# Performance work log

Hardware: AMD Instinct MI355X
Metric: run time of the kernel (lower is better)

Reference implementation:

```python
import jax, jax.numpy as jnp
import numpy as np

N = 100000  # nodes
E = 1600000  # edges


def _gcn_norm(edge_index, num_nodes):
    # PyG GCNConv default: add self-loops, symmetric normalization.
    src, dst = edge_index[0], edge_index[1]
    loop = jnp.arange(num_nodes, dtype=src.dtype)
    src = jnp.concatenate([src, loop])
    dst = jnp.concatenate([dst, loop])
    deg = jax.ops.segment_sum(jnp.ones_like(dst, dtype=jnp.float32), dst,
                              num_segments=num_nodes)
    dinv = jnp.where(deg > 0, jax.lax.rsqrt(deg), 0.0)
    norm = dinv[src] * dinv[dst]  # [E + N]
    return src, dst, norm


def _gcn_layer(x, W, b, src, dst, norm, num_nodes):
    h = x @ W                                # [N, out]
    msg = h[src] * norm[:, None]             # gather + scale, [E+N, out]
    agg = jax.ops.segment_sum(msg, dst, num_segments=num_nodes)
    return agg + b


def setup_inputs() -> dict:
    key = jax.random.key(0)
    ks = jax.random.split(key, 8)
    d_in, d_h, d_out = 128, 128, 64
    x = jax.random.normal(ks[0], (N, d_in), dtype=jnp.float32)
    edge_index = jax.random.randint(ks[1], (2, E), 0, N, dtype=jnp.int64)
    def glorot(k, fan_in, fan_out):
        s = jnp.sqrt(6.0 / (fan_in + fan_out)).astype(jnp.float32)
        return jax.random.uniform(k, (fan_in, fan_out), jnp.float32, -s, s)
    return {
        "x": x,
        "edge_index": edge_index,
        "W1": glorot(ks[2], d_in, d_h), "b1": jnp.zeros((d_h,), jnp.float32),
        "W2": glorot(ks[3], d_h, d_h), "b2": jnp.zeros((d_h,), jnp.float32),
        "W3": glorot(ks[4], d_h, d_out), "b3": jnp.zeros((d_out,), jnp.float32),
    }


def reference(x, edge_index, W1, b1, W2, b2, W3, b3):
    src, dst, norm = _gcn_norm(edge_index, N)
    h = jax.nn.relu(_gcn_layer(x, W1, b1, src, dst, norm, N))
    h = jax.nn.relu(_gcn_layer(h, W2, b2, src, dst, norm, N))
    h = jax.nn.relu(_gcn_layer(h, W3, b3, src, dst, norm, N))
    return h
```

## Files before the change

### kernel.cpp

```cpp
#include <hip/hip_runtime.h>
#include <hip/hip_bf16.h>
#include <hip/hip_fp16.h>


constexpr int N_NODES = 100000;
constexpr int E_EDGES = 1600000;
constexpr int SCAN_B = (N_NODES + 1023) / 1024;

typedef short short8 __attribute__((ext_vector_type(8)));
typedef float f32x4 __attribute__((ext_vector_type(4)));

__global__ __launch_bounds__(256) void rank_kernel(
    const int* __restrict__ dst, int* __restrict__ cnt,
    int* __restrict__ eRank) {
  int e = blockIdx.x * 256 + threadIdx.x;
  if (e < E_EDGES) eRank[e] = atomicAdd(&cnt[dst[e]], 1);
}

__global__ __launch_bounds__(256) void scan_part_kernel(
    const int* __restrict__ cnt, int* __restrict__ bsum) {
  __shared__ int red[256];
  const int t = threadIdx.x;
  int base = blockIdx.x * 1024 + t * 4;
  int4 v = make_int4(0, 0, 0, 0);
  if (base < N_NODES) v = *(const int4*)(cnt + base);
  red[t] = v.x + v.y + v.z + v.w;
  __syncthreads();
  for (int off = 128; off > 0; off >>= 1) {
    if (t < off) red[t] += red[t + off];
    __syncthreads();
  }
  if (t == 0) bsum[blockIdx.x] = red[0];
}

__global__ __launch_bounds__(128) void scan_tops_kernel(
    const int* __restrict__ bsum, int* __restrict__ boff,
    int* __restrict__ rowptr) {
  __shared__ int part[128];
  const int t = threadIdx.x;
  int v = (t < SCAN_B) ? bsum[t] : 0;
  part[t] = v;
  __syncthreads();
  for (int off = 1; off < 128; off <<= 1) {
    int add = (t >= off) ? part[t - off] : 0;
    __syncthreads();
    part[t] += add;
    __syncthreads();
  }
  if (t < SCAN_B) boff[t] = part[t] - v;
  if (t == 127) rowptr[N_NODES] = part[127];
}

__global__ __launch_bounds__(256) void scan_write_kernel(
    const int* __restrict__ cnt, const int* __restrict__ boff,
    int* __restrict__ rowptr, float* __restrict__ dinv) {
  __shared__ int part[256];
  const int t = threadIdx.x;
  int base = blockIdx.x * 1024 + t * 4;
  int4 v = make_int4(0, 0, 0, 0);
  if (base < N_NODES) v = *(const int4*)(cnt + base);
  int s = v.x + v.y + v.z + v.w;
  part[t] = s;
  __syncthreads();
  for (int off = 1; off < 256; off <<= 1) {
    int add = (t >= off) ? part[t - off] : 0;
    __syncthreads();
    part[t] += add;
    __syncthreads();
  }
  if (base < N_NODES) {
    int run = boff[blockIdx.x] + part[t] - s;
    int4 o;
    o.x = run;
    o.y = run + v.x;
    o.z = run + v.x + v.y;
    o.w = run + v.x + v.y + v.z;
    *(int4*)(rowptr + base) = o;
    float4 dv;
    dv.x = rsqrtf((float)v.x + 1.0f);
    dv.y = rsqrtf((float)v.y + 1.0f);
    dv.z = rsqrtf((float)v.z + 1.0f);
    dv.w = rsqrtf((float)v.w + 1.0f);
    *(float4*)(dinv + base) = dv;
  }
}

__global__ __launch_bounds__(256) void place_kernel(
    const int* __restrict__ src, const int* __restrict__ dst,
    const int* __restrict__ eRank, const int* __restrict__ rowptr,
    const float* __restrict__ dinv, int2* __restrict__ eSW) {
  int e = blockIdx.x * 256 + threadIdx.x;
  if (e < E_EDGES) {
    int d = dst[e];
    int s = src[e];
    int pos = rowptr[d] + eRank[e];
    eSW[pos] = make_int2(s, __float_as_int(dinv[s] * dinv[d]));
  }
}

__device__ inline ushort bf_round(float x) {
  uint u = __float_as_uint(x);
  return (ushort)((u + 0x7FFFu + ((u >> 16) & 1u)) >> 16);
}
__device__ inline ushort bf_split(float x, float* rem) {
  ushort h = bf_round(x);
  *rem = x - __uint_as_float((uint)h << 16);
  return h;
}

__device__ inline void packw_body(int id, int OC, const float* __restrict__ W,
                                  ushort* __restrict__ hi,
                                  ushort* __restrict__ lo) {
  if (id >= OC * 16) return;
  int col = id & 15;
  int g = (id >> 4) & 3;
  int ks = (id >> 6) & 3;
  int nt = id >> 8;
  int k0 = ks * 32 + g * 8;
  int n = nt * 16 + col;
  ushort h8[8], l8[8];
#pragma unroll
  for (int j = 0; j < 8; ++j) {
    float rem;
    h8[j] = bf_split(W[(size_t)(k0 + j) * OC + n], &rem);
    l8[j] = bf_round(rem);
  }
  size_t base = (size_t)id * 8;
#pragma unroll
  for (int j = 0; j < 8; ++j) {
    hi[base + j] = h8[j];
    lo[base + j] = l8[j];
  }
}

__global__ __launch_bounds__(256) void packw_all_kernel(
    const float* __restrict__ W1, ushort* __restrict__ h1,
    ushort* __restrict__ l1, const float* __restrict__ W2,
    ushort* __restrict__ h2, ushort* __restrict__ l2,
    const float* __restrict__ W3, ushort* __restrict__ h3,
    ushort* __restrict__ l3) {
  int b = blockIdx.x;
  if (b < 8) packw_body(b * 256 + threadIdx.x, 128, W1, h1, l1);
  else if (b < 16) packw_body((b - 8) * 256 + threadIdx.x, 128, W2, h2, l2);
  else packw_body((b - 16) * 256 + threadIdx.x, 64, W3, h3, l3);
}

template <int OC, bool HALF_IN>
__global__ __launch_bounds__(256) void gemm_kernel(
    const void* __restrict__ Xv, const ushort* __restrict__ Whi,
    const ushort* __restrict__ Wlo, __half* __restrict__ H) {
  constexpr int NT = OC / 16;
  __shared__ ushort sWhi[OC * 128];
  __shared__ ushort sWlo[OC * 128];
  const int t = threadIdx.x;
  {
    const uint4* gh = (const uint4*)Whi;
    const uint4* gl = (const uint4*)Wlo;
    uint4* sh = (uint4*)sWhi;
    uint4* sl = (uint4*)sWlo;
    for (int i = t; i < OC * 128 / 8; i += 256) {
      sh[i] = gh[i];
      sl[i] = gl[i];
    }
  }
  const int wid = t >> 6;
  const int lane = t & 63;
  const int bid = blockIdx.x;
  const int row = bid * 64 + wid * 16 + (lane & 15);
  const bool ok = row < N_NODES;
  const int g = lane >> 4;

  short8 ahi[4], alo[4];
#pragma unroll
  for (int ks = 0; ks < 4; ++ks) {
    float f[8];
    if (ok) {
      if constexpr (HALF_IN) {
        const __half* xr = (const __half*)Xv + (size_t)row * 128;
        uint4 u = *(const uint4*)(xr + ks * 32 + g * 8);
        float2 t0 = __half22float2(*(__half2*)&u.x);
        float2 t1 = __half22float2(*(__half2*)&u.y);
        float2 t2 = __half22float2(*(__half2*)&u.z);
        float2 t3 = __half22float2(*(__half2*)&u.w);
        f[0] = t0.x; f[1] = t0.y; f[2] = t1.x; f[3] = t1.y;
        f[4] = t2.x; f[5] = t2.y; f[6] = t3.x; f[7] = t3.y;
      } else {
        const float* xr = (const float*)Xv + (size_t)row * 128;
        float4 f0 = *(const float4*)(xr + ks * 32 + g * 8);
        float4 f1 = *(const float4*)(xr + ks * 32 + g * 8 + 4);
        f[0] = f0.x; f[1] = f0.y; f[2] = f0.z; f[3] = f0.w;
        f[4] = f1.x; f[5] = f1.y; f[6] = f1.z; f[7] = f1.w;
      }
    } else {
#pragma unroll
      for (int j = 0; j < 8; ++j) f[j] = 0.f;
    }
    union { short8 v; ushort u[8]; } h, l;
#pragma unroll
    for (int j = 0; j < 8; ++j) {
      float rem;
      h.u[j] = bf_split(f[j], &rem);
      l.u[j] = bf_round(rem);
    }
    ahi[ks] = h.v;
    alo[ks] = l.v;
  }
  __syncthreads();

#pragma unroll
  for (int nt = 0; nt < NT; ++nt) {
    f32x4 acc = {0.f, 0.f, 0.f, 0.f};
#pragma unroll
    for (int ks = 0; ks < 4; ++ks) {
      int off = (((nt * 4 + ks) * 4 + g) * 16 + (lane & 15)) * 8;
      short8 bhi = *(const short8*)&sWhi[off];
      short8 blo = *(const short8*)&sWlo[off];
      acc = __builtin_amdgcn_mfma_f32_16x16x32_bf16(alo[ks], bhi, acc, 0, 0, 0);
      acc = __builtin_amdgcn_mfma_f32_16x16x32_bf16(ahi[ks], blo, acc, 0, 0, 0);
      acc = __builtin_amdgcn_mfma_f32_16x16x32_bf16(ahi[ks], bhi, acc, 0, 0, 0);
    }
#pragma unroll
    for (int r = 0; r < 4; ++r) {
      int rr = bid * 64 + wid * 16 + g * 4 + r;
      if (rr < N_NODES)
        H[(size_t)rr * OC + nt * 16 + (lane & 15)] = __float2half(acc[r]);
    }
  }
}

template <int OC, bool HALF_OUT>
__global__ __launch_bounds__(256) void agg_kernel(
    const __half* __restrict__ H, const int* __restrict__ rowptr,
    const int2* __restrict__ eSW, const float* __restrict__ dinv,
    const float* __restrict__ bias, void* __restrict__ out) {
  const int wave = threadIdx.x >> 6;
  const int lane = threadIdx.x & 63;
  const int n = blockIdx.x * 4 + wave;
  if (n >= N_NODES) return;
  const float dn = dinv[n];
  const float selfw = dn * dn;
  const int beg = rowptr[n], end = rowptr[n + 1];
  const int jal = min(beg + (beg & 1), end);
  const int jend = jal + ((end - jal) & ~7);
  const int jend2 = jend + ((end - jend) & ~1);

  if constexpr (OC == 128) {
    const __half2* H2 = (const __half2*)H;
    float2 hv = __half22float2(H2[(size_t)n * 64 + lane]);
    float ax = hv.x * selfw, ay = hv.y * selfw;
    for (int j = beg; j < jal; ++j) {
      int2 p = eSW[j];
      float2 v = __half22float2(H2[(size_t)p.x * 64 + lane]);
      float w = __int_as_float(p.y);
      ax = fmaf(v.x, w, ax);
      ay = fmaf(v.y, w, ay);
    }
    for (int j = jal; j < jend; j += 8) {
      int4 p0 = *(const int4*)(eSW + j);
      int4 p1 = *(const int4*)(eSW + j + 2);
      int4 p2 = *(const int4*)(eSW + j + 4);
      int4 p3 = *(const int4*)(eSW + j + 6);
      __half2 h0 = H2[(size_t)p0.x * 64 + lane];
      __half2 h1 = H2[(size_t)p0.z * 64 + lane];
      __half2 h2 = H2[(size_t)p1.x * 64 + lane];
      __half2 h3 = H2[(size_t)p1.z * 64 + lane];
      __half2 h4 = H2[(size_t)p2.x * 64 + lane];
      __half2 h5 = H2[(size_t)p2.z * 64 + lane];
      __half2 h6 = H2[(size_t)p3.x * 64 + lane];
      __half2 h7 = H2[(size_t)p3.z * 64 + lane];
      float2 v0 = __half22float2(h0);
      float2 v1 = __half22float2(h1);
      float2 v2 = __half22float2(h2);
      float2 v3 = __half22float2(h3);
      float2 v4 = __half22float2(h4);
      float2 v5 = __half22float2(h5);
      float2 v6 = __half22float2(h6);
      float2 v7 = __half22float2(h7);
      ax = fmaf(v0.x, __int_as_float(p0.y), ax);
      ay = fmaf(v0.y, __int_as_float(p0.y), ay);
      ax = fmaf(v1.x, __int_as_float(p0.w), ax);
      ay = fmaf(v1.y, __int_as_float(p0.w), ay);
      ax = fmaf(v2.x, __int_as_float(p1.y), ax);
      ay = fmaf(v2.y, __int_as_float(p1.y), ay);
      ax = fmaf(v3.x, __int_as_float(p1.w), ax);
      ay = fmaf(v3.y, __int_as_float(p1.w), ay);
      ax = fmaf(v4.x, __int_as_float(p2.y), ax);
      ay = fmaf(v4.y, __int_as_float(p2.y), ay);
      ax = fmaf(v5.x, __int_as_float(p2.w), ax);
      ay = fmaf(v5.y, __int_as_float(p2.w), ay);
      ax = fmaf(v6.x, __int_as_float(p3.y), ax);
      ay = fmaf(v6.y, __int_as_float(p3.y), ay);
      ax = fmaf(v7.x, __int_as_float(p3.w), ax);
      ay = fmaf(v7.y, __int_as_float(p3.w), ay);
    }
    for (int j = jend; j < jend2; j += 2) {
      int4 p = *(const int4*)(eSW + j);
      float2 v0 = __half22float2(H2[(size_t)p.x * 64 + lane]);
      float2 v1 = __half22float2(H2[(size_t)p.z * 64 + lane]);
      ax = fmaf(v0.x, __int_as_float(p.y), ax);
      ay = fmaf(v0.y, __int_as_float(p.y), ay);
      ax = fmaf(v1.x, __int_as_float(p.w), ax);
      ay = fmaf(v1.y, __int_as_float(p.w), ay);
    }
    for (int j = jend2; j < end; ++j) {
      int2 p = eSW[j];
      float2 v = __half22float2(H2[(size_t)p.x * 64 + lane]);
      float w = __int_as_float(p.y);
      ax = fmaf(v.x, w, ax);
      ay = fmaf(v.y, w, ay);
    }
    float2 bb = ((const float2*)bias)[lane];
    float ox = fmaxf(ax + bb.x, 0.f);
    float oy = fmaxf(ay + bb.y, 0.f);
    if constexpr (HALF_OUT) {
      ((__half2*)out)[(size_t)n * 64 + lane] = __floats2half2_rn(ox, oy);
    } else {
      ((float2*)out)[(size_t)n * 64 + lane] = make_float2(ox, oy);
    }
  } else {
    float a = __half2float(H[(size_t)n * 64 + lane]) * selfw;
    for (int j = beg; j < jal; ++j) {
      int2 p = eSW[j];
      a = fmaf(__half2float(H[(size_t)p.x * 64 + lane]),
               __int_as_float(p.y), a);
    }
    for (int j = jal; j < jend; j += 8) {
      int4 p0 = *(const int4*)(eSW + j);
      int4 p1 = *(const int4*)(eSW + j + 2);
      int4 p2 = *(const int4*)(eSW + j + 4);
      int4 p3 = *(const int4*)(eSW + j + 6);
      __half h0 = H[(size_t)p0.x * 64 + lane];
      __half h1 = H[(size_t)p0.z * 64 + lane];
      __half h2 = H[(size_t)p1.x * 64 + lane];
      __half h3 = H[(size_t)p1.z * 64 + lane];
      __half h4 = H[(size_t)p2.x * 64 + lane];
      __half h5 = H[(size_t)p2.z * 64 + lane];
      __half h6 = H[(size_t)p3.x * 64 + lane];
      __half h7 = H[(size_t)p3.z * 64 + lane];
      a = fmaf(__half2float(h0), __int_as_float(p0.y), a);
      a = fmaf(__half2float(h1), __int_as_float(p0.w), a);
      a = fmaf(__half2float(h2), __int_as_float(p1.y), a);
      a = fmaf(__half2float(h3), __int_as_float(p1.w), a);
      a = fmaf(__half2float(h4), __int_as_float(p2.y), a);
      a = fmaf(__half2float(h5), __int_as_float(p2.w), a);
      a = fmaf(__half2float(h6), __int_as_float(p3.y), a);
      a = fmaf(__half2float(h7), __int_as_float(p3.w), a);
    }
    for (int j = jend; j < jend2; j += 2) {
      int4 p = *(const int4*)(eSW + j);
      a = fmaf(__half2float(H[(size_t)p.x * 64 + lane]),
               __int_as_float(p.y), a);
      a = fmaf(__half2float(H[(size_t)p.z * 64 + lane]),
               __int_as_float(p.w), a);
    }
    for (int j = jend2; j < end; ++j) {
      int2 p = eSW[j];
      a = fmaf(__half2float(H[(size_t)p.x * 64 + lane]),
               __int_as_float(p.y), a);
    }
    ((float*)out)[(size_t)n * 64 + lane] = fmaxf(a + bias[lane], 0.f);
  }
}

extern "C" void kernel_launch(void* const* d_in, const int* in_sizes, int n_in,
                              void* d_out, int out_size, void* d_ws,
                              size_t ws_size, hipStream_t stream) {
  const float* x = (const float*)d_in[0];
  const int* ei = (const int*)d_in[1];
  const float* W1 = (const float*)d_in[2];
  const float* b1 = (const float*)d_in[3];
  const float* W2 = (const float*)d_in[4];
  const float* b2 = (const float*)d_in[5];
  const float* W3 = (const float*)d_in[6];
  const float* b3 = (const float*)d_in[7];
  const int* src = ei;
  const int* dst = ei + E_EDGES;

  size_t off = 0;
  auto alloc = [&](size_t bytes) -> void* {
    void* p = (char*)d_ws + off;
    off += (bytes + 255) & ~(size_t)255;
    return p;
  };
  int* cnt = (int*)alloc((size_t)N_NODES * 4);
  int* rowptr = (int*)alloc((size_t)(N_NODES + 1) * 4);
  float* dinv = (float*)alloc((size_t)N_NODES * 4);
  int* bsum = (int*)alloc((size_t)SCAN_B * 4);
  int* boff = (int*)alloc((size_t)SCAN_B * 4);
  int* eRank = (int*)alloc((size_t)E_EDGES * 4);
  int2* eSW = (int2*)alloc((size_t)E_EDGES * 8);
  __half* h = (__half*)alloc((size_t)N_NODES * 128 * 2);
  __half* A = (__half*)alloc((size_t)N_NODES * 128 * 2);
  ushort* wp1h = (ushort*)alloc((size_t)128 * 128 * 2);
  ushort* wp1l = (ushort*)alloc((size_t)128 * 128 * 2);
  ushort* wp2h = (ushort*)alloc((size_t)128 * 128 * 2);
  ushort* wp2l = (ushort*)alloc((size_t)128 * 128 * 2);
  ushort* wp3h = (ushort*)alloc((size_t)128 * 64 * 2);
  ushort* wp3l = (ushort*)alloc((size_t)128 * 64 * 2);

  hipMemsetAsync(cnt, 0, (size_t)N_NODES * 4, stream);

  const int EB = (E_EDGES + 255) / 256;
  const int GB = (N_NODES + 63) / 64;
  const int AB = (N_NODES + 3) / 4;

  packw_all_kernel<<<20, 256, 0, stream>>>(W1, wp1h, wp1l, W2, wp2h, wp2l, W3,
                                           wp3h, wp3l);
  rank_kernel<<<EB, 256, 0, stream>>>(dst, cnt, eRank);
  gemm_kernel<128, false><<<GB, 256, 0, stream>>>(x, wp1h, wp1l, h);
  scan_part_kernel<<<SCAN_B, 256, 0, stream>>>(cnt, bsum);
  scan_tops_kernel<<<1, 128, 0, stream>>>(bsum, boff, rowptr);
  scan_write_kernel<<<SCAN_B, 256, 0, stream>>>(cnt, boff, rowptr, dinv);
  place_kernel<<<EB, 256, 0, stream>>>(src, dst, eRank, rowptr, dinv, eSW);

  agg_kernel<128, true><<<AB, 256, 0, stream>>>(h, rowptr, eSW, dinv, b1, A);
  gemm_kernel<128, true><<<GB, 256, 0, stream>>>(A, wp2h, wp2l, h);
  agg_kernel<128, true><<<AB, 256, 0, stream>>>(h, rowptr, eSW, dinv, b2, A);
  gemm_kernel<64, true><<<GB, 256, 0, stream>>>(A, wp3h, wp3l, h);
  agg_kernel<64, false><<<AB, 256, 0, stream>>>(h, rowptr, eSW, dinv, b3,
                                                d_out);
}
```

Measured before the change: 370.9 us.

## Schedule aggregation waves by degree-sorted node order; read GEMM weights from global

Builds a degree histogram during the scan, then a counting-sort permutation of nodes by in-degree, capped at 63. The aggregation kernels process nodes in that order so waves in a block get similar edge counts, reducing load imbalance. Separately, the GEMM kernel drops its LDS staging of weights, reads them straight from global/L2, and stops unrolling the output-tile loop. Costs are extra small kernels and atomics, plus scattered output writes from the permuted order, and GEMM weight loads that now depend on cache hits.

```diff
diff --git a/kernel.cpp b/kernel.cpp
--- a/kernel.cpp
+++ b/kernel.cpp
@@ -18,12 +18,22 @@
 }
 
 __global__ __launch_bounds__(256) void scan_part_kernel(
-    const int* __restrict__ cnt, int* __restrict__ bsum) {
+    const int* __restrict__ cnt, int* __restrict__ bsum,
+    int* __restrict__ dhist) {
   __shared__ int red[256];
+  __shared__ int lh[64];
   const int t = threadIdx.x;
+  if (t < 64) lh[t] = 0;
+  __syncthreads();
   int base = blockIdx.x * 1024 + t * 4;
   int4 v = make_int4(0, 0, 0, 0);
-  if (base < N_NODES) v = *(const int4*)(cnt + base);
+  if (base < N_NODES) {
+    v = *(const int4*)(cnt + base);
+    atomicAdd(&lh[min(v.x, 63)], 1);
+    atomicAdd(&lh[min(v.y, 63)], 1);
+    atomicAdd(&lh[min(v.z, 63)], 1);
+    atomicAdd(&lh[min(v.w, 63)], 1);
+  }
   red[t] = v.x + v.y + v.z + v.w;
   __syncthreads();
   for (int off = 128; off > 0; off >>= 1) {
@@ -31,6 +41,7 @@
     __syncthreads();
   }
   if (t == 0) bsum[blockIdx.x] = red[0];
+  if (t < 64 && lh[t]) atomicAdd(&dhist[t], lh[t]);
 }
 
 __global__ __launch_bounds__(128) void scan_tops_kernel(
@@ -49,6 +60,18 @@
   }
   if (t < SCAN_B) boff[t] = part[t] - v;
   if (t == 127) rowptr[N_NODES] = part[127];
+}
+
+__global__ __launch_bounds__(64) void dscan_kernel(
+    const int* __restrict__ dhist, int* __restrict__ dbase) {
+  const int t = threadIdx.x;
+  int h = dhist[t];
+  int v = h;
+  for (int off = 1; off < 64; off <<= 1) {
+    int u = __shfl_up(v, off);
+    if (t >= off) v += u;
+  }
+  dbase[t] = v - h;
 }
 
 __global__ __launch_bounds__(256) void scan_write_kernel(
@@ -85,6 +108,16 @@
   }
 }
 
+__global__ __launch_bounds__(256) void dperm_kernel(
+    const int* __restrict__ cnt, const int* __restrict__ dbase,
+    int* __restrict__ dcur, int* __restrict__ perm) {
+  int n = blockIdx.x * 256 + threadIdx.x;
+  if (n < N_NODES) {
+    int d = min(cnt[n], 63);
+    perm[dbase[d] + atomicAdd(&dcur[d], 1)] = n;
+  }
+}
+
 __global__ __launch_bounds__(256) void place_kernel(
     const int* __restrict__ src, const int* __restrict__ dst,
     const int* __restrict__ eRank, const int* __restrict__ rowptr,
@@ -150,19 +183,7 @@
     const void* __restrict__ Xv, const ushort* __restrict__ Whi,
     const ushort* __restrict__ Wlo, __half* __restrict__ H) {
   constexpr int NT = OC / 16;
-  __shared__ ushort sWhi[OC * 128];
-  __shared__ ushort sWlo[OC * 128];
   const int t = threadIdx.x;
-  {
-    const uint4* gh = (const uint4*)Whi;
-    const uint4* gl = (const uint4*)Wlo;
-    uint4* sh = (uint4*)sWhi;
-    uint4* sl = (uint4*)sWlo;
-    for (int i = t; i < OC * 128 / 8; i += 256) {
-      sh[i] = gh[i];
-      sl[i] = gl[i];
-    }
-  }
   const int wid = t >> 6;
   const int lane = t & 63;
   const int bid = blockIdx.x;
@@ -205,16 +226,15 @@
     ahi[ks] = h.v;
     alo[ks] = l.v;
   }
-  __syncthreads();
-
-#pragma unroll
+
+#pragma unroll 1
   for (int nt = 0; nt < NT; ++nt) {
     f32x4 acc = {0.f, 0.f, 0.f, 0.f};
 #pragma unroll
     for (int ks = 0; ks < 4; ++ks) {
       int off = (((nt * 4 + ks) * 4 + g) * 16 + (lane & 15)) * 8;
-      short8 bhi = *(const short8*)&sWhi[off];
-      short8 blo = *(const short8*)&sWlo[off];
+      short8 bhi = *(const short8*)&Whi[off];
+      short8 blo = *(const short8*)&Wlo[off];
       acc = __builtin_amdgcn_mfma_f32_16x16x32_bf16(alo[ks], bhi, acc, 0, 0, 0);
       acc = __builtin_amdgcn_mfma_f32_16x16x32_bf16(ahi[ks], blo, acc, 0, 0, 0);
       acc = __builtin_amdgcn_mfma_f32_16x16x32_bf16(ahi[ks], bhi, acc, 0, 0, 0);
@@ -232,11 +252,13 @@
 __global__ __launch_bounds__(256) void agg_kernel(
     const __half* __restrict__ H, const int* __restrict__ rowptr,
     const int2* __restrict__ eSW, const float* __restrict__ dinv,
-    const float* __restrict__ bias, void* __restrict__ out) {
+    const float* __restrict__ bias, const int* __restrict__ perm,
+    void* __restrict__ out) {
   const int wave = threadIdx.x >> 6;
   const int lane = threadIdx.x & 63;
-  const int n = blockIdx.x * 4 + wave;
-  if (n >= N_NODES) return;
+  const int unit = blockIdx.x * 4 + wave;
+  if (unit >= N_NODES) return;
+  const int n = perm[unit];
   const float dn = dinv[n];
   const float selfw = dn * dn;
   const int beg = rowptr[n], end = rowptr[n + 1];
@@ -387,6 +409,11 @@
   float* dinv = (float*)alloc((size_t)N_NODES * 4);
   int* bsum = (int*)alloc((size_t)SCAN_B * 4);
   int* boff = (int*)alloc((size_t)SCAN_B * 4);
+  int* dstat = (int*)alloc((size_t)192 * 4);
+  int* dhist = dstat;
+  int* dcur = dstat + 64;
+  int* dbase = dstat + 128;
+  int* perm = (int*)alloc((size_t)N_NODES * 4);
   int* eRank = (int*)alloc((size_t)E_EDGES * 4);
   int2* eSW = (int2*)alloc((size_t)E_EDGES * 8);
   __half* h = (__half*)alloc((size_t)N_NODES * 128 * 2);
@@ -399,8 +426,10 @@
   ushort* wp3l = (ushort*)alloc((size_t)128 * 64 * 2);
 
   hipMemsetAsync(cnt, 0, (size_t)N_NODES * 4, stream);
+  hipMemsetAsync(dstat, 0, (size_t)128 * 4, stream);
 
   const int EB = (E_EDGES + 255) / 256;
+  const int NB = (N_NODES + 255) / 256;
   const int GB = (N_NODES + 63) / 64;
   const int AB = (N_NODES + 3) / 4;
 
@@ -408,15 +437,19 @@
                                            wp3h, wp3l);
   rank_kernel<<<EB, 256, 0, stream>>>(dst, cnt, eRank);
   gemm_kernel<128, false><<<GB, 256, 0, stream>>>(x, wp1h, wp1l, h);
-  scan_part_kernel<<<SCAN_B, 256, 0, stream>>>(cnt, bsum);
+  scan_part_kernel<<<SCAN_B, 256, 0, stream>>>(cnt, bsum, dhist);
   scan_tops_kernel<<<1, 128, 0, stream>>>(bsum, boff, rowptr);
+  dscan_kernel<<<1, 64, 0, stream>>>(dhist, dbase);
   scan_write_kernel<<<SCAN_B, 256, 0, stream>>>(cnt, boff, rowptr, dinv);
+  dperm_kernel<<<NB, 256, 0, stream>>>(cnt, dbase, dcur, perm);
   place_kernel<<<EB, 256, 0, stream>>>(src, dst, eRank, rowptr, dinv, eSW);
 
-  agg_kernel<128, true><<<AB, 256, 0, stream>>>(h, rowptr, eSW, dinv, b1, A);
+  agg_kernel<128, true><<<AB, 256, 0, stream>>>(h, rowptr, eSW, dinv, b1,
+                                                perm, A);
   gemm_kernel<128, true><<<GB, 256, 0, stream>>>(A, wp2h, wp2l, h);
-  agg_kernel<128, true><<<AB, 256, 0, stream>>>(h, rowptr, eSW, dinv, b2, A);
+  agg_kernel<128, true><<<AB, 256, 0, stream>>>(h, rowptr, eSW, dinv, b2,
+                                                perm, A);
   gemm_kernel<64, true><<<GB, 256, 0, stream>>>(A, wp3h, wp3l, h);
   agg_kernel<64, false><<<AB, 256, 0, stream>>>(h, rowptr, eSW, dinv, b3,
-                                                d_out);
-}
+                                                perm, d_out);
+}
```

Result: slower. 654.1 us (+76.4%).
